# Kernel optimization log

Hardware: AMD Instinct MI355X
Metric: run time of the kernel (lower is better)

## Reference

```python
import jax, jax.numpy as jnp
import numpy as np

N_NODES = 50000
N_EDGES = 800000
F_IN = 256
HEADS = 8
OUT_CH = 10  # hard-coded in the source GATv2Conv(in, 10, heads=H)
HIDDEN = HEADS * OUT_CH  # 80
NEG_SLOPE = 0.2  # PyG GATv2Conv default


def _gatv2_layer(x, src, dst, Wl, Wr, att, b, n):
    """One GATv2Conv layer (eval mode, concat=True, self-loops already added).
    x: [n, F_in]; src/dst: [E_tot] int; Wl/Wr: [F_in, H*C]; att: [H, C]; b: [H*C].
    """
    xl = (x @ Wl).reshape(n, HEADS, OUT_CH)  # source-side transform
    xr = (x @ Wr).reshape(n, HEADS, OUT_CH)  # target-side transform
    # gather -> LeakyReLU -> attention logit per edge/head
    e = jax.nn.leaky_relu(xl[src] + xr[dst], NEG_SLOPE)      # [E, H, C]
    logits = jnp.einsum('ehc,hc->eh', e, att)                # [E, H]
    # segment softmax over incoming edges of each target node
    m = jax.ops.segment_max(logits, dst, num_segments=n)     # [n, H]
    ex = jnp.exp(logits - m[dst])
    denom = jax.ops.segment_sum(ex, dst, num_segments=n)     # [n, H]
    alpha = ex / (denom[dst] + 1e-16)                        # [E, H]
    # scatter-add aggregation of weighted source messages
    out = jax.ops.segment_sum(xl[src] * alpha[:, :, None], dst, num_segments=n)
    return out.reshape(n, HIDDEN) + b


def _gat_forward(x, edge_index, params):
    n = x.shape[0]
    loops = jnp.arange(n, dtype=edge_index.dtype)
    src = jnp.concatenate([edge_index[0], loops])  # add self loops (PyG default)
    dst = jnp.concatenate([edge_index[1], loops])
    for (Wl, Wr, att, b) in params:
        x = jax.nn.elu(_gatv2_layer(x, src, dst, Wl, Wr, att, b, n))
    return x


def setup_inputs() -> dict:
    key = jax.random.key(0)
    ks = jax.random.split(key, 16)
    x = jax.random.normal(ks[0], (N_NODES, F_IN), dtype=jnp.float32)
    edge_index = jax.random.randint(ks[1], (2, N_EDGES), 0, N_NODES, dtype=jnp.int64)
    inp = {'x': x, 'edge_index': edge_index}
    dims_in = [F_IN, HIDDEN, HIDDEN]
    for i, d_in in enumerate(dims_in):
        k0, k1, k2 = jax.random.split(ks[2 + i], 3)
        s = 1.0 / np.sqrt(d_in)
        inp[f'Wl{i}'] = jax.random.normal(k0, (d_in, HIDDEN), dtype=jnp.float32) * s
        inp[f'Wr{i}'] = jax.random.normal(k1, (d_in, HIDDEN), dtype=jnp.float32) * s
        inp[f'att{i}'] = jax.random.normal(k2, (HEADS, OUT_CH), dtype=jnp.float32) * 0.1
        inp[f'b{i}'] = jnp.zeros((HIDDEN,), dtype=jnp.float32)
    return inp


def reference(x, edge_index, Wl0, Wr0, att0, b0, Wl1, Wr1, att1, b1, Wl2, Wr2, att2, b2):
    params = [(Wl0, Wr0, att0, b0), (Wl1, Wr1, att1, b1), (Wl2, Wr2, att2, b2)]
    return _gat_forward(x, edge_index, params)
```

## Files before the change

kernel.cpp:

```cpp
#include <hip/hip_runtime.h>
#include <math.h>

#define N_NODES 50000
#define N_EDGES 800000
#define E_TOT   (N_EDGES + N_NODES)
#define HEADS   8
#define OUTC    10
#define HID     80
#define NEG_SLOPE 0.2f


__global__ __launch_bounds__(256) void hist_k(const int* __restrict__ ei, int* __restrict__ cnt) {
    int e = blockIdx.x * blockDim.x + threadIdx.x;
    if (e >= E_TOT) return;
    int d = (e < N_EDGES) ? ei[N_EDGES + e] : (e - N_EDGES);
    atomicAdd(&cnt[d], 1);
}

__global__ __launch_bounds__(1024) void scan_k(const int* __restrict__ cnt, int* __restrict__ rowptr) {
    __shared__ int wsum[16];
    __shared__ int carry_s;
    const int tid = threadIdx.x;
    const int lane = tid & 63, wid = tid >> 6;
    if (tid == 0) carry_s = 0;
    __syncthreads();
    for (int base = 0; base < N_NODES; base += 1024) {
        int i = base + tid;
        int v = (i < N_NODES) ? cnt[i] : 0;
        int s = v;
        #pragma unroll
        for (int off = 1; off < 64; off <<= 1) {
            int t = __shfl_up(s, off, 64);
            if (lane >= off) s += t;
        }
        if (lane == 63) wsum[wid] = s;
        int carry = carry_s;
        __syncthreads();
        if (wid == 0 && lane < 16) {
            int w = wsum[lane];
            #pragma unroll
            for (int off = 1; off < 16; off <<= 1) {
                int t = __shfl_up(w, off, 16);
                if (lane >= off) w += t;
            }
            wsum[lane] = w;
        }
        __syncthreads();
        int woff = (wid > 0) ? wsum[wid - 1] : 0;
        int incl = s + woff;
        int excl = incl - v;
        if (i < N_NODES) rowptr[i] = carry + excl;
        int total = wsum[15];
        __syncthreads();
        if (tid == 0) carry_s = carry + total;
        __syncthreads();
    }
    if (tid == 0) rowptr[N_NODES] = carry_s;
}

__global__ __launch_bounds__(256) void scatter_k(const int* __restrict__ ei,
                                                 const int* __restrict__ rowptr,
                                                 int* __restrict__ cursor,
                                                 int* __restrict__ csr) {
    int e = blockIdx.x * blockDim.x + threadIdx.x;
    if (e >= E_TOT) return;
    int s, d;
    if (e < N_EDGES) { s = ei[e]; d = ei[N_EDGES + e]; }
    else { s = e - N_EDGES; d = s; }
    int pos = rowptr[d] + atomicAdd(&cursor[d], 1);
    csr[pos] = s;
}


#define KC 32
__global__ __launch_bounds__(256) void gemm_k(const float* __restrict__ A, int K,
                                              const float* __restrict__ Wl,
                                              const float* __restrict__ Wr,
                                              float* __restrict__ xl,
                                              float* __restrict__ xr) {
    __shared__ float sa[64][KC + 1];
    __shared__ float sw[KC][160];
    const int tid = threadIdx.x;
    const int rg = tid & 15;
    const int cg = tid >> 4;
    const int row0 = blockIdx.x * 64;

    float acc[4][10];
    #pragma unroll
    for (int r = 0; r < 4; ++r)
        #pragma unroll
        for (int j = 0; j < 10; ++j) acc[r][j] = 0.f;

    for (int kb = 0; kb < K; kb += KC) {
        #pragma unroll
        for (int it = 0; it < 2; ++it) {
            int idx = tid + it * 256;
            int r = idx >> 3, k4 = idx & 7;
            int grow = row0 + r, gk = kb + k4 * 4;
            float4 v = make_float4(0.f, 0.f, 0.f, 0.f);
            if (grow < N_NODES && gk < K)
                v = *reinterpret_cast<const float4*>(A + (size_t)grow * K + gk);
            sa[r][k4 * 4 + 0] = v.x; sa[r][k4 * 4 + 1] = v.y;
            sa[r][k4 * 4 + 2] = v.z; sa[r][k4 * 4 + 3] = v.w;
        }
        for (int idx = tid; idx < KC * 40; idx += 256) {
            int k = idx / 40, c4 = idx % 40;
            int gk = kb + k, c = c4 * 4;
            float4 v = make_float4(0.f, 0.f, 0.f, 0.f);
            if (gk < K) {
                if (c < 80) v = *reinterpret_cast<const float4*>(Wl + (size_t)gk * 80 + c);
                else        v = *reinterpret_cast<const float4*>(Wr + (size_t)gk * 80 + (c - 80));
            }
            sw[k][c + 0] = v.x; sw[k][c + 1] = v.y; sw[k][c + 2] = v.z; sw[k][c + 3] = v.w;
        }
        __syncthreads();
        #pragma unroll 4
        for (int k = 0; k < KC; ++k) {
            float a0 = sa[rg * 4 + 0][k];
            float a1 = sa[rg * 4 + 1][k];
            float a2 = sa[rg * 4 + 2][k];
            float a3 = sa[rg * 4 + 3][k];
            #pragma unroll
            for (int j = 0; j < 10; ++j) {
                float w = sw[k][cg * 10 + j];
                acc[0][j] = fmaf(a0, w, acc[0][j]);
                acc[1][j] = fmaf(a1, w, acc[1][j]);
                acc[2][j] = fmaf(a2, w, acc[2][j]);
                acc[3][j] = fmaf(a3, w, acc[3][j]);
            }
        }
        __syncthreads();
    }
    const int c = cg * 10;
    float* basep = (c < 80) ? xl : xr;
    const int cc = (c < 80) ? c : (c - 80);
    #pragma unroll
    for (int r = 0; r < 4; ++r) {
        int grow = row0 + rg * 4 + r;
        if (grow >= N_NODES) continue;
        float* dstp = basep + (size_t)grow * HID + cc;
        #pragma unroll
        for (int j = 0; j < 10; ++j) dstp[j] = acc[r][j];
    }
}


__global__ __launch_bounds__(256) void agg_k(const float* __restrict__ xl,
                                             const float* __restrict__ xr,
                                             const int* __restrict__ rowptr,
                                             const int* __restrict__ csr,
                                             const float* __restrict__ att,
                                             const float* __restrict__ bias,
                                             float* __restrict__ out) {
    const int tid = threadIdx.x;
    const int lane = tid & 63;
    const int node = blockIdx.x * 4 + (tid >> 6);
    if (node >= N_NODES) return;
    const int g = lane >> 4;
    const int u = lane & 15;
    const int cb = u * 5;

    float att5[5], xr5[5];
    #pragma unroll
    for (int c = 0; c < 5; ++c) {
        att5[c] = att[cb + c];
        xr5[c] = xr[(size_t)node * HID + cb + c];
    }
    const int ro = rowptr[node];
    const int deg = rowptr[node + 1] - ro;

    float m = -INFINITY, s = 0.f;
    float acc[5] = {0.f, 0.f, 0.f, 0.f, 0.f};

    for (int i = g; i < deg; i += 4) {
        const int src = csr[ro + i];
        const float* xlp = xl + (size_t)src * HID + cb;
        float xl5[5];
        float part = 0.f;
        #pragma unroll
        for (int c = 0; c < 5; ++c) {
            xl5[c] = xlp[c];
            float e = xl5[c] + xr5[c];
            e = (e > 0.f) ? e : NEG_SLOPE * e;
            part = fmaf(e, att5[c], part);
        }
        const float logit = part + __shfl_xor(part, 1, 64);
        const float nm = fmaxf(m, logit);
        const float scale = __expf(m - nm);
        const float p = __expf(logit - nm);
        s = s * scale + p;
        #pragma unroll
        for (int c = 0; c < 5; ++c) acc[c] = acc[c] * scale + p * xl5[c];
        m = nm;
    }

    #pragma unroll
    for (int off = 16; off <= 32; off <<= 1) {
        const float om = __shfl_xor(m, off, 64);
        const float os = __shfl_xor(s, off, 64);
        float oacc[5];
        #pragma unroll
        for (int c = 0; c < 5; ++c) oacc[c] = __shfl_xor(acc[c], off, 64);
        const float nm = fmaxf(m, om);
        const float sc1 = (m == -INFINITY) ? 0.f : __expf(m - nm);
        const float sc2 = (om == -INFINITY) ? 0.f : __expf(om - nm);
        s = s * sc1 + os * sc2;
        #pragma unroll
        for (int c = 0; c < 5; ++c) acc[c] = acc[c] * sc1 + oacc[c] * sc2;
        m = nm;
    }

    if (g == 0) {
        const float inv = 1.f / (s + 1e-16f);
        #pragma unroll
        for (int c = 0; c < 5; ++c) {
            float v = acc[c] * inv + bias[cb + c];
            v = (v > 0.f) ? v : (__expf(v) - 1.f);
            out[(size_t)node * HID + cb + c] = v;
        }
    }
}


extern "C" void kernel_launch(void* const* d_in, const int* in_sizes, int n_in,
                              void* d_out, int out_size, void* d_ws, size_t ws_size,
                              hipStream_t stream) {
    const float* x  = (const float*)d_in[0];
    const int*   ei = (const int*)d_in[1];
    const float* Wl[3]   = {(const float*)d_in[2], (const float*)d_in[6],  (const float*)d_in[10]};
    const float* Wr[3]   = {(const float*)d_in[3], (const float*)d_in[7],  (const float*)d_in[11]};
    const float* attp[3] = {(const float*)d_in[4], (const float*)d_in[8],  (const float*)d_in[12]};
    const float* bp[3]   = {(const float*)d_in[5], (const float*)d_in[9],  (const float*)d_in[13]};

    char* ws = (char*)d_ws;
    size_t off = 0;
    auto alloc = [&](size_t bytes) -> void* {
        void* p = ws + off;
        off += (bytes + 255) & ~(size_t)255;
        return p;
    };
    int* cnt    = (int*)alloc((size_t)N_NODES * 4);
    int* cursor = (int*)alloc((size_t)N_NODES * 4);
    int* rowptr = (int*)alloc((size_t)(N_NODES + 1) * 4);
    int* csr    = (int*)alloc((size_t)E_TOT * 4);
    float* xl   = (float*)alloc((size_t)N_NODES * HID * 4);
    float* xr   = (float*)alloc((size_t)N_NODES * HID * 4);
    float* actA = (float*)alloc((size_t)N_NODES * HID * 4);
    float* actB = (float*)alloc((size_t)N_NODES * HID * 4);

    hipMemsetAsync(cnt, 0, (size_t)N_NODES * 4, stream);
    hipMemsetAsync(cursor, 0, (size_t)N_NODES * 4, stream);

    hist_k<<<(E_TOT + 255) / 256, 256, 0, stream>>>(ei, cnt);
    scan_k<<<1, 1024, 0, stream>>>(cnt, rowptr);
    scatter_k<<<(E_TOT + 255) / 256, 256, 0, stream>>>(ei, rowptr, cursor, csr);

    for (int l = 0; l < 3; ++l) {
        const float* act_in = (l == 0) ? x : (l == 1 ? actA : actB);
        const int K = (l == 0) ? 256 : 80;
        gemm_k<<<(N_NODES + 63) / 64, 256, 0, stream>>>(act_in, K, Wl[l], Wr[l], xl, xr);
        float* out_l = (l == 0) ? actA : (l == 1 ? actB : (float*)d_out);
        agg_k<<<N_NODES / 4, 256, 0, stream>>>(xl, xr, rowptr, csr, attp[l], bp[l], out_l);
    }
}
```

Before: 542.2 us.

## Replace shared-memory tiled GEMM with register-only row-per-lane GEMM

Rewrites the node feature transform so each lane owns one row and each wave computes 20 output columns, with weights read as wave-uniform float4 loads (broadcast/scalar path) and activations read directly from global memory. This removes LDS staging and the barriers around it, and writes outputs as float4. In exchange, each lane streams its own row with strided float4 loads that coalesce poorly across the wave. The same A row is also re-read by the four waves and by the two column-half blocks, which relies on cache reuse.

```diff
diff --git a/kernel.cpp b/kernel.cpp
--- a/kernel.cpp
+++ b/kernel.cpp
@@ -72,75 +72,52 @@
 }
 
 
-#define KC 32
-__global__ __launch_bounds__(256) void gemm_k(const float* __restrict__ A, int K,
-                                              const float* __restrict__ Wl,
-                                              const float* __restrict__ Wr,
-                                              float* __restrict__ xl,
-                                              float* __restrict__ xr) {
-    __shared__ float sa[64][KC + 1];
-    __shared__ float sw[KC][160];
-    const int tid = threadIdx.x;
-    const int rg = tid & 15;
-    const int cg = tid >> 4;
-    const int row0 = blockIdx.x * 64;
-
-    float acc[4][10];
+#define TC 20
+__global__ __launch_bounds__(256) void gemm2_k(const float* __restrict__ A, int K,
+                                               const float* __restrict__ Wl,
+                                               const float* __restrict__ Wr,
+                                               float* __restrict__ xl,
+                                               float* __restrict__ xr) {
+    const int lane = threadIdx.x & 63;
+    const int wv = __builtin_amdgcn_readfirstlane(threadIdx.x >> 6);
+    const int rg = blockIdx.x >> 1;
+    const int cb = blockIdx.x & 1;
+    const int row = rg * 64 + lane;
+    const int j0 = wv * TC;
+
+    const float* __restrict__ W = cb ? Wr : Wl;
+    float* __restrict__ Xo = cb ? xr : xl;
+
+    const int r = (row < N_NODES) ? row : (N_NODES - 1);
+    const float* __restrict__ Ar = A + (size_t)r * K;
+
+    float acc[TC];
     #pragma unroll
-    for (int r = 0; r < 4; ++r)
-        #pragma unroll
-        for (int j = 0; j < 10; ++j) acc[r][j] = 0.f;
-
-    for (int kb = 0; kb < K; kb += KC) {
-        #pragma unroll
-        for (int it = 0; it < 2; ++it) {
-            int idx = tid + it * 256;
-            int r = idx >> 3, k4 = idx & 7;
-            int grow = row0 + r, gk = kb + k4 * 4;
-            float4 v = make_float4(0.f, 0.f, 0.f, 0.f);
-            if (grow < N_NODES && gk < K)
-                v = *reinterpret_cast<const float4*>(A + (size_t)grow * K + gk);
-            sa[r][k4 * 4 + 0] = v.x; sa[r][k4 * 4 + 1] = v.y;
-            sa[r][k4 * 4 + 2] = v.z; sa[r][k4 * 4 + 3] = v.w;
-        }
-        for (int idx = tid; idx < KC * 40; idx += 256) {
-            int k = idx / 40, c4 = idx % 40;
-            int gk = kb + k, c = c4 * 4;
-            float4 v = make_float4(0.f, 0.f, 0.f, 0.f);
-            if (gk < K) {
-                if (c < 80) v = *reinterpret_cast<const float4*>(Wl + (size_t)gk * 80 + c);
-                else        v = *reinterpret_cast<const float4*>(Wr + (size_t)gk * 80 + (c - 80));
+    for (int j = 0; j < TC; ++j) acc[j] = 0.f;
+
+    for (int kb = 0; kb < K; kb += 4) {
+        const float4 a = *reinterpret_cast<const float4*>(Ar + kb);
+        #pragma unroll
+        for (int t = 0; t < 4; ++t) {
+            const float av = (t == 0) ? a.x : (t == 1) ? a.y : (t == 2) ? a.z : a.w;
+            const float* __restrict__ wrow = W + (size_t)(kb + t) * HID + j0;
+            #pragma unroll
+            for (int q = 0; q < 5; ++q) {
+                const float4 w = *reinterpret_cast<const float4*>(wrow + q * 4);
+                acc[q * 4 + 0] = fmaf(av, w.x, acc[q * 4 + 0]);
+                acc[q * 4 + 1] = fmaf(av, w.y, acc[q * 4 + 1]);
+                acc[q * 4 + 2] = fmaf(av, w.z, acc[q * 4 + 2]);
+                acc[q * 4 + 3] = fmaf(av, w.w, acc[q * 4 + 3]);
             }
-            sw[k][c + 0] = v.x; sw[k][c + 1] = v.y; sw[k][c + 2] = v.z; sw[k][c + 3] = v.w;
-        }
-        __syncthreads();
-        #pragma unroll 4
-        for (int k = 0; k < KC; ++k) {
-            float a0 = sa[rg * 4 + 0][k];
-            float a1 = sa[rg * 4 + 1][k];
-            float a2 = sa[rg * 4 + 2][k];
-            float a3 = sa[rg * 4 + 3][k];
-            #pragma unroll
-            for (int j = 0; j < 10; ++j) {
-                float w = sw[k][cg * 10 + j];
-                acc[0][j] = fmaf(a0, w, acc[0][j]);
-                acc[1][j] = fmaf(a1, w, acc[1][j]);
-                acc[2][j] = fmaf(a2, w, acc[2][j]);
-                acc[3][j] = fmaf(a3, w, acc[3][j]);
-            }
-        }
-        __syncthreads();
-    }
-    const int c = cg * 10;
-    float* basep = (c < 80) ? xl : xr;
-    const int cc = (c < 80) ? c : (c - 80);
-    #pragma unroll
-    for (int r = 0; r < 4; ++r) {
-        int grow = row0 + rg * 4 + r;
-        if (grow >= N_NODES) continue;
-        float* dstp = basep + (size_t)grow * HID + cc;
-        #pragma unroll
-        for (int j = 0; j < 10; ++j) dstp[j] = acc[r][j];
+        }
+    }
+
+    if (row < N_NODES) {
+        float* op = Xo + (size_t)row * HID + j0;
+        #pragma unroll
+        for (int q = 0; q < 5; ++q)
+            *reinterpret_cast<float4*>(op + q * 4) =
+                make_float4(acc[q * 4 + 0], acc[q * 4 + 1], acc[q * 4 + 2], acc[q * 4 + 3]);
     }
 }
 
@@ -258,7 +235,7 @@
     for (int l = 0; l < 3; ++l) {
         const float* act_in = (l == 0) ? x : (l == 1 ? actA : actB);
         const int K = (l == 0) ? 256 : 80;
-        gemm_k<<<(N_NODES + 63) / 64, 256, 0, stream>>>(act_in, K, Wl[l], Wr[l], xl, xr);
+        gemm2_k<<<1564, 256, 0, stream>>>(act_in, K, Wl[l], Wr[l], xl, xr);
         float* out_l = (l == 0) ? actA : (l == 1 ? actB : (float*)d_out);
         agg_k<<<N_NODES / 4, 256, 0, stream>>>(xl, xr, rowptr, csr, attp[l], bp[l], out_l);
     }
```

New measurement: 506.2 us. -6.6%, faster.
